# Performance work log

Measured on AMD Instinct MI355X. Metric: run time of the kernel, lower is better.

The kernel has to match this reference:

```python
import jax, jax.numpy as jnp
import numpy as np

TEMPERATURE = 0.1
GAMMA = 0.5
LOSS_WEIGHT = 1.0
N, D = 8192, 64
EPS_COS = 1e-8
EPS_NCE = 1e-6
SQ_EPS = 1e-12  # (1e-6 distance)^2


def setup_inputs() -> dict:
    key = jax.random.key(0)
    k1, k2, k3 = jax.random.split(key, 3)
    features = jax.random.normal(k1, (N, D), dtype=jnp.float32)
    labels = jax.random.randint(k2, (N,), 0, 3, dtype=jnp.int64)
    coords = jax.random.uniform(k3, (N, 3), dtype=jnp.float32)
    return {"features": features, "labels": labels, "coords": coords}


def reference(features, labels, coords):
    # line-point mask (label == 2); pairwise math on the masked subset is
    # expressed as full pairwise + (m_i & m_j) masking, mathematically
    # identical to extract-then-pairwise in the torch original.
    m = labels == 2                       # [N] bool
    mf = m.astype(features.dtype)
    L = jnp.sum(mf)                       # number of line points

    # cosine similarity: normalize then GEMM (== F.cosine_similarity pairwise)
    norm = jnp.maximum(jnp.linalg.norm(features, axis=1, keepdims=True), EPS_COS)
    fn = features / norm
    feat_sim = fn @ fn.T                  # [N, N]

    # squared pairwise coordinate distances (cdist^2), clamped >= 0
    sq_norm = jnp.sum(coords * coords, axis=1)
    sq = sq_norm[:, None] + sq_norm[None, :] - 2.0 * (coords @ coords.T)
    sq = jnp.maximum(sq, 0.0)             # [N, N]

    pair = m[:, None] & m[None, :]
    within = (sq < 1.0) & (sq > SQ_EPS)   # dist < 1.0 and dist > 1e-6
    pos = pair & within
    neg = pair & ~within                  # original neg_mask = ~pos over subset

    posf = pos.astype(feat_sim.dtype)
    negf = neg.astype(feat_sim.dtype)

    exp_sim = jnp.exp(feat_sim / TEMPERATURE)
    sum_exp = jnp.sum(exp_sim * negf, axis=1)
    pos_sum = jnp.sum(exp_sim * posf, axis=1)
    ratio = pos_sum / (sum_exp + pos_sum + EPS_NCE)
    # mean of -log(ratio) over line points only (guard non-line rows)
    per_point = -jnp.log(jnp.where(m, ratio, 1.0))
    info_nce = jnp.sum(per_point * mf) / L

    # continuity: mean over the L x L subset matrix of |(1 - sim) - dist| * pos
    safe_sq = jnp.where(pos, sq, 1.0)     # avoid sqrt(0) NaN grads on masked entries
    coord_dist = jnp.sqrt(safe_sq)
    continuity = jnp.sum(jnp.abs((1.0 - feat_sim) - coord_dist) * posf) / (L * L)

    return (info_nce + GAMMA * continuity) * LOSS_WEIGHT
```

## Files before the change

kernel.cpp:

```cpp
#include <hip/hip_runtime.h>
#include <math.h>


typedef short s16x8 __attribute__((ext_vector_type(8)));
typedef float f32x4 __attribute__((ext_vector_type(4)));

#define NPTS 8192
#define DIM 64
#define BT 128
#define GRID_P 512
#define PSTRIDE 4096
#define MAXSLOT 32

#define OFF_L 0
#define OFF_IDX 1024
#define OFF_FH (OFF_IDX + NPTS * 4)
#define OFF_FL (OFF_FH + NPTS * DIM * 2)
#define OFF_CS (OFF_FL + NPTS * DIM * 2)
#define OFF_DF (OFF_CS + NPTS * 16)
#define OFF_PP (OFF_DF + NPTS * 4)
#define OFF_PN (OFF_PP + MAXSLOT * PSTRIDE * 4)
#define OFF_CT (OFF_PN + MAXSLOT * PSTRIDE * 4)

__global__ __launch_bounds__(1024) void k_scan(const int* __restrict__ labels,
                                               int* __restrict__ idx,
                                               int* __restrict__ Lout) {
  __shared__ int wres[16];
  __shared__ int wsum[16];
  const int t = threadIdx.x;
  const int lane = t & 63;
  const int wid = t >> 6;
  const int base = t * 8;
  int w[8];
#pragma unroll
  for (int j = 0; j < 8; j++) w[j] = labels[base + j];
  int oddz = (w[1] == 0) && (w[3] == 0) && (w[5] == 0) && (w[7] == 0);
  unsigned long long wa = __ballot(!oddz);
  if (lane == 0) wres[wid] = (wa == 0ull);
  __syncthreads();
  int is64 = 1;
#pragma unroll
  for (int i = 0; i < 16; i++) is64 &= wres[i];

  int bits = 0, cnt = 0;
  if (is64) {
    const long long* l64 = (const long long*)labels;
#pragma unroll
    for (int j = 0; j < 8; j++) {
      bool f = (l64[base + j] == 2ll);
      bits |= ((int)f) << j;
      cnt += (int)f;
    }
  } else {
#pragma unroll
    for (int j = 0; j < 8; j++) {
      bool f = (w[j] == 2);
      bits |= ((int)f) << j;
      cnt += (int)f;
    }
  }
  int inc = cnt;
#pragma unroll
  for (int m = 1; m < 64; m <<= 1) {
    int v = __shfl_up(inc, m);
    if (lane >= m) inc += v;
  }
  if (lane == 63) wsum[wid] = inc;
  __syncthreads();
  if (t < 16) {
    int v = wsum[t];
    int sc = v;
#pragma unroll
    for (int m = 1; m < 16; m <<= 1) {
      int u = __shfl_up(sc, m);
      if (t >= m) sc += u;
    }
    wsum[t] = sc - v;
    if (t == 15) *Lout = sc;
  }
  __syncthreads();
  int pos = wsum[wid] + inc - cnt;
#pragma unroll
  for (int j = 0; j < 8; j++) {
    if (bits & (1 << j)) idx[pos++] = base + j;
  }
}

__global__ __launch_bounds__(256) void k_gather(const float* __restrict__ feats,
                                                const float* __restrict__ coords,
                                                const int* __restrict__ idx,
                                                const int* __restrict__ Lp,
                                                ushort* __restrict__ fnHi,
                                                ushort* __restrict__ fnLo,
                                                float4* __restrict__ cs,
                                                int* __restrict__ diagf) {
  const int L = *Lp;
  const int gw = (int)((blockIdx.x * blockDim.x + threadIdx.x) >> 6);
  const int lane = threadIdx.x & 63;
  if (gw >= L) {
    fnHi[gw * 64 + lane] = 0;
    fnLo[gw * 64 + lane] = 0;
    return;
  }
  const int row = idx[gw];
  float f = feats[row * DIM + lane];
  float ss = f * f;
#pragma unroll
  for (int m = 32; m; m >>= 1) ss += __shfl_xor(ss, m);
  float nrm = fmaxf(sqrtf(ss), 1e-8f);
  float fn = f / nrm;
  unsigned int u = __float_as_uint(fn);
  unsigned int hb = (u + 0x7FFFu + ((u >> 16) & 1u)) >> 16;
  float hif = __uint_as_float(hb << 16);
  float lof = fn - hif;
  unsigned int ul = __float_as_uint(lof);
  unsigned int lb = (ul + 0x7FFFu + ((ul >> 16) & 1u)) >> 16;
  fnHi[gw * 64 + lane] = (ushort)hb;
  fnLo[gw * 64 + lane] = (ushort)lb;
  if (lane == 0) {
    float c0 = coords[row * 3 + 0];
    float c1 = coords[row * 3 + 1];
    float c2 = coords[row * 3 + 2];
    float p0 = __fmul_rn(c0, c0);
    float p1 = __fmul_rn(c1, c1);
    float p2 = __fmul_rn(c2, c2);
    float s = __fadd_rn(__fadd_rn(p0, p1), p2);
    float g = __fadd_rn(__fadd_rn(p0, p2), p1);
    diagf[gw] = (__fadd_rn(s, -g) > 5e-13f) ? 1 : 0;
    cs[gw] = make_float4(c0, c1, c2, c0 * c0 + c1 * c1 + c2 * c2);
  }
}

__global__ __launch_bounds__(256, 2) void k_pair(const ushort* __restrict__ fnHi,
                                                 const ushort* __restrict__ fnLo,
                                                 const float4* __restrict__ cs,
                                                 const int* __restrict__ Lp,
                                                 const int* __restrict__ diagf,
                                                 float* __restrict__ pp,
                                                 float* __restrict__ pn,
                                                 float* __restrict__ contp) {
  __shared__ ushort AB[4][128][72];
  __shared__ float cred[4];

  const int L = *Lp;
  const int nT = (L + BT - 1) >> 7;
  const int nItems = nT * nT;
  const int t = threadIdx.x;
  const int lane = t & 63, wid = t >> 6;
  const int m = lane & 15;
  const int koct = lane >> 4;
  float cont = 0.f;

  for (int wi = blockIdx.x; wi < nItems; wi += GRID_P) {
    const int bi = wi / nT;
    const int jt = wi - bi * nT;
    const int rb = bi << 7, cb = jt << 7;

    __syncthreads();
#pragma unroll
    for (int i = 0; i < 16; i++) {
      int q = t + 256 * i;
      int sel = q >> 10;
      int row = (q >> 3) & 127;
      int oct = q & 7;
      int slot = ((sel < 2) ? rb : cb) + row;
      const ushort* src = (sel & 1) ? fnLo : fnHi;
      s16x8 v = *(const s16x8*)&src[slot * 64 + oct * 8];
      *(s16x8*)&AB[sel][row][oct * 8] = v;
    }
    __syncthreads();

    f32x4 acc[2][8];
#pragma unroll
    for (int rt = 0; rt < 2; rt++)
#pragma unroll
      for (int ct = 0; ct < 8; ct++) acc[rt][ct] = (f32x4){0.f, 0.f, 0.f, 0.f};

#pragma unroll
    for (int kk = 0; kk < 2; kk++) {
      const int kof = kk * 32 + koct * 8;
      s16x8 ah[2], al[2], bh[8], bl[8];
#pragma unroll
      for (int rt = 0; rt < 2; rt++) {
        ah[rt] = *(const s16x8*)&AB[0][wid * 32 + rt * 16 + m][kof];
        al[rt] = *(const s16x8*)&AB[1][wid * 32 + rt * 16 + m][kof];
      }
#pragma unroll
      for (int ct = 0; ct < 8; ct++) {
        bh[ct] = *(const s16x8*)&AB[2][ct * 16 + m][kof];
        bl[ct] = *(const s16x8*)&AB[3][ct * 16 + m][kof];
      }
#pragma unroll
      for (int rt = 0; rt < 2; rt++)
#pragma unroll
        for (int ct = 0; ct < 8; ct++) {
          acc[rt][ct] = __builtin_amdgcn_mfma_f32_16x16x32_bf16(ah[rt], bh[ct], acc[rt][ct], 0, 0, 0);
          acc[rt][ct] = __builtin_amdgcn_mfma_f32_16x16x32_bf16(ah[rt], bl[ct], acc[rt][ct], 0, 0, 0);
          acc[rt][ct] = __builtin_amdgcn_mfma_f32_16x16x32_bf16(al[rt], bh[ct], acc[rt][ct], 0, 0, 0);
        }
    }

    float4 crow[2][4];
    int dfr[2][4];
#pragma unroll
    for (int rt = 0; rt < 2; rt++)
#pragma unroll
      for (int rg = 0; rg < 4; rg++) {
        int ig = rb + wid * 32 + rt * 16 + koct * 4 + rg;
        crow[rt][rg] = cs[ig];
        dfr[rt][rg] = diagf[ig];
      }
    float pos_r[2][4] = {{0.f, 0.f, 0.f, 0.f}, {0.f, 0.f, 0.f, 0.f}};
    float neg_r[2][4] = {{0.f, 0.f, 0.f, 0.f}, {0.f, 0.f, 0.f, 0.f}};
#pragma unroll
    for (int ct = 0; ct < 8; ct++) {
      int jg = cb + ct * 16 + m;
      float4 cbv = cs[jg];
      bool jv = (jg < L);
#pragma unroll
      for (int rt = 0; rt < 2; rt++)
#pragma unroll
        for (int rg = 0; rg < 4; rg++) {
          int ig = rb + wid * 32 + rt * 16 + koct * 4 + rg;
          bool valid = jv && (ig < L);
          float sim = acc[rt][ct][rg];
          float4 cav = crow[rt][rg];
          float d3 = cav.x * cbv.x + cav.y * cbv.y + cav.z * cbv.z;
          float sq = fmaxf(cav.w + cbv.w - 2.f * d3, 0.f);
          bool within = (sq < 1.0f) && (sq > 1e-12f);
          if (ig == jg) within = (dfr[rt][rg] != 0);
          float e = __expf(sim * 10.f);
          if (valid) {
            if (within) {
              pos_r[rt][rg] += e;
              cont += fabsf(1.f - sim - sqrtf(sq));
            } else {
              neg_r[rt][rg] += e;
            }
          }
        }
    }
#pragma unroll
    for (int rt = 0; rt < 2; rt++)
#pragma unroll
      for (int rg = 0; rg < 4; rg++) {
        float p = pos_r[rt][rg], n = neg_r[rt][rg];
#pragma unroll
        for (int s = 1; s < 16; s <<= 1) {
          p += __shfl_xor(p, s);
          n += __shfl_xor(n, s);
        }
        if (m == 0) {
          int ig = rb + wid * 32 + rt * 16 + koct * 4 + rg;
          pp[jt * PSTRIDE + ig] = p;
          pn[jt * PSTRIDE + ig] = n;
        }
      }
  }

#pragma unroll
  for (int s = 1; s < 64; s <<= 1) cont += __shfl_xor(cont, s);
  if (lane == 0) cred[wid] = cont;
  __syncthreads();
  if (t == 0) contp[blockIdx.x] = cred[0] + cred[1] + cred[2] + cred[3];
}

__global__ __launch_bounds__(1024) void k_final(const float* __restrict__ pp,
                                                const float* __restrict__ pn,
                                                const float* __restrict__ contp,
                                                const int* __restrict__ Lp,
                                                float* __restrict__ out) {
  __shared__ float red[32];
  const int L = *Lp;
  const int nslots = (L + BT - 1) >> 7;
  const int t = threadIdx.x;
  float accI = 0.f;
  for (int s = t; s < L; s += 1024) {
    float pos = 0.f, neg = 0.f;
    for (int c = 0; c < nslots; c++) {
      pos += pp[c * PSTRIDE + s];
      neg += pn[c * PSTRIDE + s];
    }
    accI += -logf(pos / (neg + pos + 1e-6f));
  }
  float accC = 0.f;
  for (int c = t; c < GRID_P; c += 1024) accC += contp[c];
#pragma unroll
  for (int m = 1; m < 64; m <<= 1) {
    accI += __shfl_xor(accI, m);
    accC += __shfl_xor(accC, m);
  }
  if ((t & 63) == 0) {
    red[t >> 6] = accI;
    red[16 + (t >> 6)] = accC;
  }
  __syncthreads();
  if (t == 0) {
    float sI = 0.f, sC = 0.f;
#pragma unroll
    for (int w = 0; w < 16; w++) {
      sI += red[w];
      sC += red[16 + w];
    }
    float fL = (float)L;
    out[0] = sI / fL + 0.5f * (sC / (fL * fL));
  }
}

extern "C" void kernel_launch(void* const* d_in, const int* in_sizes, int n_in,
                              void* d_out, int out_size, void* d_ws, size_t ws_size,
                              hipStream_t stream) {
  const float* features = (const float*)d_in[0];
  const int* labels = (const int*)d_in[1];
  const float* coords = (const float*)d_in[2];

  char* ws = (char*)d_ws;
  int* Lp = (int*)(ws + OFF_L);
  int* idx = (int*)(ws + OFF_IDX);
  ushort* fnHi = (ushort*)(ws + OFF_FH);
  ushort* fnLo = (ushort*)(ws + OFF_FL);
  float4* cs = (float4*)(ws + OFF_CS);
  int* diagf = (int*)(ws + OFF_DF);
  float* pp = (float*)(ws + OFF_PP);
  float* pn = (float*)(ws + OFF_PN);
  float* contp = (float*)(ws + OFF_CT);
  float* out = (float*)d_out;

  k_scan<<<1, 1024, 0, stream>>>(labels, idx, Lp);
  k_gather<<<(NPTS * 64) / 256, 256, 0, stream>>>(features, coords, idx, Lp, fnHi, fnLo, cs, diagf);
  k_pair<<<GRID_P, 256, 0, stream>>>(fnHi, fnLo, cs, Lp, diagf, pp, pn, contp);
  k_final<<<1, 1024, 0, stream>>>(pp, pn, contp, Lp, out);
}
```

Measured before the change: 47.94 us.

## Halve LDS tile by staging K in two chunks; raise occupancy to three blocks

```diff
diff --git a/kernel.cpp b/kernel.cpp
--- a/kernel.cpp
+++ b/kernel.cpp
@@ -100,6 +100,10 @@
   if (gw >= L) {
     fnHi[gw * 64 + lane] = 0;
     fnLo[gw * 64 + lane] = 0;
+    if (lane == 0) {
+      cs[gw] = make_float4(0.f, 0.f, 0.f, 0.f);
+      diagf[gw] = 0;
+    }
     return;
   }
   const int row = idx[gw];
@@ -109,12 +113,12 @@
   for (int m = 32; m; m >>= 1) ss += __shfl_xor(ss, m);
   float nrm = fmaxf(sqrtf(ss), 1e-8f);
   float fn = f / nrm;
-  unsigned int u = __float_as_uint(fn);
-  unsigned int hb = (u + 0x7FFFu + ((u >> 16) & 1u)) >> 16;
+  unsigned u = __float_as_uint(fn);
+  unsigned hb = (u + 0x7FFFu + ((u >> 16) & 1u)) >> 16;
   float hif = __uint_as_float(hb << 16);
   float lof = fn - hif;
-  unsigned int ul = __float_as_uint(lof);
-  unsigned int lb = (ul + 0x7FFFu + ((ul >> 16) & 1u)) >> 16;
+  unsigned ul = __float_as_uint(lof);
+  unsigned lb = (ul + 0x7FFFu + ((ul >> 16) & 1u)) >> 16;
   fnHi[gw * 64 + lane] = (ushort)hb;
   fnLo[gw * 64 + lane] = (ushort)lb;
   if (lane == 0) {
@@ -131,7 +135,7 @@
   }
 }
 
-__global__ __launch_bounds__(256, 2) void k_pair(const ushort* __restrict__ fnHi,
+__global__ __launch_bounds__(256, 3) void k_pair(const ushort* __restrict__ fnHi,
                                                  const ushort* __restrict__ fnLo,
                                                  const float4* __restrict__ cs,
                                                  const int* __restrict__ Lp,
@@ -139,7 +143,7 @@
                                                  float* __restrict__ pp,
                                                  float* __restrict__ pn,
                                                  float* __restrict__ contp) {
-  __shared__ ushort AB[4][128][72];
+  __shared__ __attribute__((aligned(16))) ushort AB[4][128][40];
   __shared__ float cred[4];
 
   const int L = *Lp;
@@ -154,22 +158,9 @@
   for (int wi = blockIdx.x; wi < nItems; wi += GRID_P) {
     const int bi = wi / nT;
     const int jt = wi - bi * nT;
+    const bool isDiag = (bi == jt);
     const int rb = bi << 7, cb = jt << 7;
 
-    __syncthreads();
-#pragma unroll
-    for (int i = 0; i < 16; i++) {
-      int q = t + 256 * i;
-      int sel = q >> 10;
-      int row = (q >> 3) & 127;
-      int oct = q & 7;
-      int slot = ((sel < 2) ? rb : cb) + row;
-      const ushort* src = (sel & 1) ? fnLo : fnHi;
-      s16x8 v = *(const s16x8*)&src[slot * 64 + oct * 8];
-      *(s16x8*)&AB[sel][row][oct * 8] = v;
-    }
-    __syncthreads();
-
     f32x4 acc[2][8];
 #pragma unroll
     for (int rt = 0; rt < 2; rt++)
@@ -178,17 +169,31 @@
 
 #pragma unroll
     for (int kk = 0; kk < 2; kk++) {
-      const int kof = kk * 32 + koct * 8;
+      __syncthreads();
+#pragma unroll
+      for (int i = 0; i < 8; i++) {
+        int q = t + 256 * i;
+        int sel = q >> 9;
+        int row = (q >> 2) & 127;
+        int oct = q & 3;
+        int slot = ((sel < 2) ? rb : cb) + row;
+        const ushort* src = (sel & 1) ? fnLo : fnHi;
+        s16x8 v = *(const s16x8*)&src[slot * 64 + kk * 32 + oct * 8];
+        *(s16x8*)&AB[sel][row][oct * 8] = v;
+      }
+      __syncthreads();
+
+      const int kofd = koct * 8;
       s16x8 ah[2], al[2], bh[8], bl[8];
 #pragma unroll
       for (int rt = 0; rt < 2; rt++) {
-        ah[rt] = *(const s16x8*)&AB[0][wid * 32 + rt * 16 + m][kof];
-        al[rt] = *(const s16x8*)&AB[1][wid * 32 + rt * 16 + m][kof];
+        ah[rt] = *(const s16x8*)&AB[0][wid * 32 + rt * 16 + m][kofd];
+        al[rt] = *(const s16x8*)&AB[1][wid * 32 + rt * 16 + m][kofd];
       }
 #pragma unroll
       for (int ct = 0; ct < 8; ct++) {
-        bh[ct] = *(const s16x8*)&AB[2][ct * 16 + m][kof];
-        bl[ct] = *(const s16x8*)&AB[3][ct * 16 + m][kof];
+        bh[ct] = *(const s16x8*)&AB[2][ct * 16 + m][kofd];
+        bl[ct] = *(const s16x8*)&AB[3][ct * 16 + m][kofd];
       }
 #pragma unroll
       for (int rt = 0; rt < 2; rt++)
@@ -208,7 +213,7 @@
       for (int rg = 0; rg < 4; rg++) {
         int ig = rb + wid * 32 + rt * 16 + koct * 4 + rg;
         crow[rt][rg] = cs[ig];
-        dfr[rt][rg] = diagf[ig];
+        dfr[rt][rg] = isDiag ? diagf[ig] : 0;
       }
     float pos_r[2][4] = {{0.f, 0.f, 0.f, 0.f}, {0.f, 0.f, 0.f, 0.f}};
     float neg_r[2][4] = {{0.f, 0.f, 0.f, 0.f}, {0.f, 0.f, 0.f, 0.f}};
@@ -228,7 +233,7 @@
           float d3 = cav.x * cbv.x + cav.y * cbv.y + cav.z * cbv.z;
           float sq = fmaxf(cav.w + cbv.w - 2.f * d3, 0.f);
           bool within = (sq < 1.0f) && (sq > 1e-12f);
-          if (ig == jg) within = (dfr[rt][rg] != 0);
+          if (isDiag && ig == jg) within = (dfr[rt][rg] != 0);
           float e = __expf(sim * 10.f);
           if (valid) {
             if (within) {
@@ -246,9 +251,9 @@
       for (int rg = 0; rg < 4; rg++) {
         float p = pos_r[rt][rg], n = neg_r[rt][rg];
 #pragma unroll
-        for (int s = 1; s < 16; s <<= 1) {
-          p += __shfl_xor(p, s);
-          n += __shfl_xor(n, s);
+        for (int s1 = 1; s1 < 16; s1 <<= 1) {
+          p += __shfl_xor(p, s1);
+          n += __shfl_xor(n, s1);
         }
         if (m == 0) {
           int ig = rb + wid * 32 + rt * 16 + koct * 4 + rg;
@@ -259,7 +264,8 @@
   }
 
 #pragma unroll
-  for (int s = 1; s < 64; s <<= 1) cont += __shfl_xor(cont, s);
+  for (int s1 = 1; s1 < 64; s1 <<= 1) cont += __shfl_xor(cont, s1);
+  __syncthreads();
   if (lane == 0) cred[wid] = cont;
   __syncthreads();
   if (t == 0) contp[blockIdx.x] = cred[0] + cred[1] + cred[2] + cred[3];
```

After: 49.84 us. 4.0% more time.
